# Optimization experiments

Measured on AMD Instinct MI355X. Metric: run time of the kernel, lower is better.

Reference implementation:

```python
import jax, jax.numpy as jnp
import numpy as np

T, N, D, E, L = 3, 50000, 64, 800000, 2


def setup_inputs() -> dict:
    key = jax.random.key(0)
    ks = jax.random.split(key, 12)
    glorot = lambda k, shape: jax.random.uniform(
        k, shape, jnp.float32, -1.0, 1.0) * np.sqrt(6.0 / (shape[-2] + shape[-1]))
    return {
        "x": jax.random.normal(ks[0], (N, D), jnp.float32),
        "edge_index": jax.random.randint(ks[1], (2, E), 0, N),
        "edge_type": jax.random.randint(ks[2], (E,), 0, T),
        "edge_feature": jax.random.normal(ks[3], (T, D), jnp.float32),
        # per-layer parameters stacked along leading L axis
        "theta_g": glorot(ks[4], (L, T, D)),
        "theta_hi": glorot(ks[5], (L, T, D)),
        "theta_hj": glorot(ks[6], (L, T, D)),
        "we": glorot(ks[7], (L, D, D)),
        "wr": glorot(ks[8], (L, D, D)),
    }


def _scatter_softmax(r, row, n):
    # r: [T,E], softmax over edges grouped by destination node `row`
    rT = r.T  # [E,T]
    m = jax.ops.segment_max(rT, row, num_segments=n)  # [N,T]
    e = jnp.exp(rT - m[row])
    s = jax.ops.segment_sum(e, row, num_segments=n)
    return (e / s[row]).T  # [T,E]


def _layer(x, ef, tg, thi, thj, we, wr, row, col, etype, n):
    # attention logits per edge, per type-slice
    r_g = jnp.einsum('ed,td->te', ef, tg)[:, etype]          # [T,E]
    r_hi = jnp.einsum('tnd,td->tn', x, thi)[:, row]          # [T,E]
    r_hj = jnp.einsum('tnd,td->tn', x, thj)[:, col]          # [T,E]
    r = _scatter_softmax(r_g + r_hi + r_hj, row, n)          # [T,E]
    ef_new = ef @ wr                                         # [et,D]
    v = jax.nn.sigmoid(ef_new)[etype][None] * (x @ we)[:, col]  # [T,E,D]
    out = r[..., None] * v                                   # [T,E,D]
    out = jax.ops.segment_sum(out.transpose(1, 0, 2), row, num_segments=n)
    return out.transpose(1, 0, 2), ef_new                    # [T,N,D]


def reference(x, edge_index, edge_type, edge_feature, theta_g, theta_hi, theta_hj, we, wr):
    row, col = edge_index[0], edge_index[1]
    h = jnp.broadcast_to(x[None], (T, N, D))
    ef = edge_feature
    for i in range(L):
        h_prev = h
        out, ef = _layer(h, ef, theta_g[i], theta_hi[i], theta_hj[i],
                         we[i], wr[i], row, col, edge_type, N)
        if i == L - 1:
            h = out
            break
        h = h_prev + jax.nn.relu(out)  # dropout p=0 -> identity
        ef = jax.nn.relu(ef)
    return h
```

## Files before the change

### kernel.cpp

```cpp
#include <hip/hip_runtime.h>
#include <math.h>

#define TT 3
#define NN 50000
#define DD 64
#define EE 800000
#define LL 2
#define NK3 (NN * TT)
#define CH 96
#define NBC ((EE + 255) / 256)
#define NBM ((NN + 63) / 64)
#define NBKT ((NN + 127) / 128)
#define KPB 384
#define HP 3136

typedef _Float16 h4 __attribute__((ext_vector_type(4)));
typedef float f4 __attribute__((ext_vector_type(4)));

__global__ __launch_bounds__(256) void k_fusedA(
    const int* __restrict__ row, const int* __restrict__ et,
    int* __restrict__ blockHistT,
    const float* __restrict__ x,
    const float* __restrict__ we,
    const float* __restrict__ thj,
    _Float16* __restrict__ hw0,
    float* __restrict__ ahj0,
    const float* __restrict__ ef0,
    const float* __restrict__ tg,
    const float* __restrict__ wr,
    float* __restrict__ rg,
    float* __restrict__ sig,
    _Float16* __restrict__ bf)
{
    __shared__ _Float16 Ah[64][68];
    __shared__ _Float16 Bt[80][68];
    __shared__ int lhist[NBKT];
    int b = blockIdx.x, tid = threadIdx.x;

    if (b < NBC) {
        for (int i = tid; i < NBKT; i += 256) lhist[i] = 0;
        __syncthreads();
        int e = b * 256 + tid;
        int bkt = row[e] >> 7;
        atomicAdd(&lhist[bkt], 1);
        __syncthreads();
        for (int i = tid; i < NBKT; i += 256)
            blockHistT[(size_t)i * HP + b] = lhist[i];
        return;
    }
    if (b < NBC + NBM) {
        long rbase = (long)(b - NBC) * 64;
        #pragma unroll
        for (int it = 0; it < 4; ++it) {
            int flat = (tid + it * 256) * 4;
            int r = flat >> 6, k = flat & 63;
            h4 hv = {};
            if (rbase + r < NN) {
                float4 v = *(const float4*)&x[(rbase + r) * 64 + k];
                hv = h4{ (_Float16)v.x, (_Float16)v.y, (_Float16)v.z, (_Float16)v.w };
            }
            *(h4*)&Ah[r][k] = hv;
        }
        for (int idx = tid; idx < 80 * 64; idx += 256) {
            int c = idx >> 6, k = idx & 63;
            float v = 0.f;
            if (c < 64) v = we[k * 64 + c];
            else if (c < 67) v = thj[(c - 64) * 64 + k];
            Bt[c][k] = (_Float16)v;
        }
        __syncthreads();
        int wid = tid >> 6, lane = tid & 63;
        int r16 = lane & 15, kq = lane >> 4;
        f4 acc[5] = {};
        #pragma unroll
        for (int ks = 0; ks < 4; ++ks) {
            int k0 = ks * 16 + kq * 4;
            h4 a = *(h4*)&Ah[wid * 16 + r16][k0];
            #pragma unroll
            for (int ct = 0; ct < 5; ++ct) {
                h4 bb = *(h4*)&Bt[ct * 16 + r16][k0];
                acc[ct] = __builtin_amdgcn_mfma_f32_16x16x16f16(a, bb, acc[ct], 0, 0, 0);
            }
        }
        #pragma unroll
        for (int j = 0; j < 4; ++j) {
            long g = rbase + wid * 16 + kq * 4 + j;
            if (g < NN) {
                #pragma unroll
                for (int ct = 0; ct < 4; ++ct)
                    hw0[g * 64 + ct * 16 + r16] = (_Float16)acc[ct][j];
                if (r16 < 3) ahj0[g * 4 + r16] = acc[4][j];
            }
        }
        return;
    }
    float* ef_l = (float*)&Ah[0][0];
    float* efn  = ef_l + TT * DD;
    for (int l = 0; l < LL; ++l)
        for (int idx = tid; idx < 80 * 64; idx += 256) {
            int c = idx >> 6, k = idx & 63;
            float v = 0.f;
            if (c < 64) v = we[l * 4096 + k * 64 + c];
            else if (c < 67) v = thj[l * 192 + (c - 64) * 64 + k];
            bf[l * 5120 + idx] = (_Float16)v;
        }
    if (tid < TT * DD) ef_l[tid] = ef0[tid];
    __syncthreads();
    for (int layer = 0; layer < LL; ++layer) {
        if (tid < TT * TT) {
            int t = tid / TT, tau = tid % TT;
            float s = 0.f;
            #pragma unroll
            for (int k = 0; k < DD; ++k)
                s += ef_l[tau * DD + k] * tg[layer * TT * DD + t * DD + k];
            rg[layer * TT * TT + tid] = s;
        }
        if (tid < TT * DD) {
            int tau = tid / DD, d = tid % DD;
            float s = 0.f;
            #pragma unroll
            for (int k = 0; k < DD; ++k)
                s += ef_l[tau * DD + k] * wr[layer * DD * DD + k * DD + d];
            efn[tid] = s;
            sig[layer * TT * DD + tid] = 1.f / (1.f + expf(-s));
        }
        __syncthreads();
        if (tid < TT * DD) ef_l[tid] = fmaxf(efn[tid], 0.f);
        __syncthreads();
    }
}

__global__ __launch_bounds__(256) void k_colscan(
    int* __restrict__ blockHistT, int* __restrict__ bucketTotal)
{
    __shared__ int sc[256];
    __shared__ int carryB;
    int j = blockIdx.x, tid = threadIdx.x;
    int* colp = blockHistT + (size_t)j * HP;
    if (tid == 0) carryB = 0;
    __syncthreads();
    for (int c0 = 0; c0 < NBC; c0 += 256) {
        int b = c0 + tid;
        int v = (b < NBC) ? colp[b] : 0;
        sc[tid] = v;
        __syncthreads();
        for (int off = 1; off < 256; off <<= 1) {
            int u = (tid >= off) ? sc[tid - off] : 0;
            __syncthreads();
            sc[tid] += u;
            __syncthreads();
        }
        int cb = carryB;
        if (b < NBC) colp[b] = cb + sc[tid] - v;
        __syncthreads();
        if (tid == 0) carryB = cb + sc[255];
        __syncthreads();
    }
    if (tid == 0) bucketTotal[j] = carryB;
}

__global__ __launch_bounds__(256) void k_bucket(
    const int* __restrict__ row, const int* __restrict__ et,
    const int* __restrict__ col,
    const int* __restrict__ bucketTotal,
    const int* __restrict__ blockOffT,
    unsigned* __restrict__ bucketed)
{
    __shared__ int lrank[NBKT];
    __shared__ int lbase[NBKT];
    __shared__ int sc[256];
    __shared__ int carryC;
    int b = blockIdx.x, tid = threadIdx.x;
    for (int i = tid; i < NBKT; i += 256) lrank[i] = 0;
    if (tid == 0) carryC = 0;
    __syncthreads();
    for (int c0 = 0; c0 < NBKT; c0 += 256) {
        int i = c0 + tid;
        int v = (i < NBKT) ? bucketTotal[i] : 0;
        sc[tid] = v;
        __syncthreads();
        for (int off = 1; off < 256; off <<= 1) {
            int u = (tid >= off) ? sc[tid - off] : 0;
            __syncthreads();
            sc[tid] += u;
            __syncthreads();
        }
        int cb = carryC;
        if (i < NBKT) lbase[i] = cb + sc[tid] - v;
        __syncthreads();
        if (tid == 0) carryC = cb + sc[255];
        __syncthreads();
    }
    int e = b * 256 + tid;
    int r = row[e], tt = et[e], c = col[e];
    int bkt = r >> 7;
    int kl = (r - (bkt << 7)) * 3 + tt;
    int rk = atomicAdd(&lrank[bkt], 1);
    int pos = lbase[bkt] + blockOffT[(size_t)bkt * HP + b] + rk;
    bucketed[pos] = ((unsigned)kl << 16) | (unsigned)c;
}

__global__ __launch_bounds__(256) void k_emit3(
    const unsigned* __restrict__ bucketed,
    const int* __restrict__ bucketTotal,
    int* __restrict__ csroff,
    unsigned short* __restrict__ pk)
{
    __shared__ int counts[KPB];
    __shared__ int csr[KPB];
    __shared__ int sc[256];
    __shared__ int carryS;
    int j = blockIdx.x, tid = threadIdx.x;
    int pp = 0;
    for (int i = tid; i < j; i += 256) pp += bucketTotal[i];
    sc[tid] = pp;
    __syncthreads();
    for (int off = 128; off >= 1; off >>= 1) {
        if (tid < off) sc[tid] += sc[tid + off];
        __syncthreads();
    }
    int base = sc[0];
    int tot = bucketTotal[j];
    __syncthreads();
    for (int k = tid; k < KPB; k += 256) counts[k] = 0;
    if (tid == 0) carryS = 0;
    __syncthreads();
    for (int i = tid; i < tot; i += 256) {
        int kl = (int)(bucketed[base + i] >> 16);
        atomicAdd(&counts[kl], 1);
    }
    __syncthreads();
    for (int c0 = 0; c0 < KPB; c0 += 256) {
        int k = c0 + tid;
        int v = (k < KPB) ? counts[k] : 0;
        sc[tid] = v;
        __syncthreads();
        for (int off = 1; off < 256; off <<= 1) {
            int u = (tid >= off) ? sc[tid - off] : 0;
            __syncthreads();
            sc[tid] += u;
            __syncthreads();
        }
        int cb = carryS;
        if (k < KPB) csr[k] = cb + sc[tid] - v;
        __syncthreads();
        if (tid == 0) carryS = cb + sc[255];
        __syncthreads();
    }
    for (int k = tid; k < KPB; k += 256) {
        int gk = j * KPB + k;
        if (gk <= NK3) csroff[gk] = base + csr[k];
    }
    for (int k = tid; k < KPB; k += 256) counts[k] = 0;
    __syncthreads();
    for (int i = tid; i < tot; i += 256) {
        unsigned rec = bucketed[base + i];
        int kl = (int)(rec >> 16);
        int rk = atomicAdd(&counts[kl], 1);
        pk[base + csr[kl] + rk] = (unsigned short)(rec & 0xFFFFu);
    }
}

__global__ __launch_bounds__(256) void k_mm1(
    const _Float16* __restrict__ h,
    const _Float16* __restrict__ Bf,
    _Float16* __restrict__ hw,
    float* __restrict__ ahj)
{
    __shared__ _Float16 Ah[64][68];
    __shared__ _Float16 Bt[80][68];
    int tid = threadIdx.x;
    long rbase = (long)blockIdx.x * 64;

    #pragma unroll
    for (int it = 0; it < 4; ++it) {
        int flat = (tid + it * 256) * 4;
        int r = flat >> 6, k = flat & 63;
        h4 hv = {};
        if (rbase + r < NK3) hv = *(const h4*)&h[(rbase + r) * 64 + k];
        *(h4*)&Ah[r][k] = hv;
    }
    for (int e4 = tid; e4 < 80 * 64 / 4; e4 += 256) {
        int idx = e4 * 4;
        *(h4*)&Bt[idx >> 6][idx & 63] = *(const h4*)&Bf[idx];
    }
    __syncthreads();

    int wid = tid >> 6, lane = tid & 63;
    int r16 = lane & 15, kq = lane >> 4;
    f4 acc[5] = {};
    #pragma unroll
    for (int ks = 0; ks < 4; ++ks) {
        int k0 = ks * 16 + kq * 4;
        h4 a = *(h4*)&Ah[wid * 16 + r16][k0];
        #pragma unroll
        for (int ct = 0; ct < 5; ++ct) {
            h4 b = *(h4*)&Bt[ct * 16 + r16][k0];
            acc[ct] = __builtin_amdgcn_mfma_f32_16x16x16f16(a, b, acc[ct], 0, 0, 0);
        }
    }
    #pragma unroll
    for (int j = 0; j < 4; ++j) {
        long g = rbase + wid * 16 + kq * 4 + j;
        if (g < NK3) {
            int t = (g >= 2L * NN) ? 2 : (g >= NN ? 1 : 0);
            long n = g - (long)t * NN;
            #pragma unroll
            for (int ct = 0; ct < 4; ++ct)
                hw[((size_t)n * 3 + t) * 64 + ct * 16 + r16] = (_Float16)acc[ct][j];
            if (r16 == t) ahj[n * 4 + t] = acc[4][j];
        }
    }
}

__global__ __launch_bounds__(256) void k_edge0(
    const int* __restrict__ off3,
    const unsigned short* __restrict__ pk,
    const float* __restrict__ rg_l,
    const float* __restrict__ sig_l,
    const float* __restrict__ ahj4,
    const _Float16* __restrict__ hw,
    const float* __restrict__ x,
    _Float16* __restrict__ outh)
{
    __shared__ uint4 ent[4][CH];
    int wid = threadIdx.x >> 6, lane = threadIdx.x & 63;
    int n = blockIdx.x * 4 + wid;
    int b3 = n * 3;
    int s0 = off3[b3], s1 = off3[b3 + 1], s2 = off3[b3 + 2], s3 = off3[b3 + 3];
    float r00 = rg_l[0], r01 = rg_l[1], r02 = rg_l[2];
    float r10 = rg_l[3], r11 = rg_l[4], r12 = rg_l[5];
    float r20 = rg_l[6], r21 = rg_l[7], r22 = rg_l[8];
    float sg0 = sig_l[lane], sg1 = sig_l[64 + lane], sg2 = sig_l[128 + lane];
    const char* hwb = (const char*)hw + (size_t)lane * 2;
    uint4* myent = ent[wid];
    float acc0 = 0.f, acc1 = 0.f, acc2 = 0.f;
    float ps0 = 0.f, ps1 = 0.f, ps2 = 0.f;

    for (int base = s0; base < s3; base += CH) {
        int cnt = s3 - base; if (cnt > CH) cnt = CH;
        for (int jj = lane; jj < cnt; jj += 64) {
            int ei = base + jj;
            int c = pk[ei];
            int tau = (ei >= s1) + (ei >= s2);
            float4 aj = *(const float4*)&ahj4[c * 4];
            float g0 = (tau == 0) ? r00 : ((tau == 1) ? r01 : r02);
            float g1 = (tau == 0) ? r10 : ((tau == 1) ? r11 : r12);
            float g2 = (tau == 0) ? r20 : ((tau == 1) ? r21 : r22);
            float p0 = __expf(g0 + aj.x);
            float p1 = __expf(g1 + aj.y);
            float p2 = __expf(g2 + aj.z);
            ps0 += p0; ps1 += p1; ps2 += p2;
            myent[jj] = make_uint4(((unsigned)c * 128u) | ((unsigned)tau << 26),
                                   __float_as_uint(p0), __float_as_uint(p1),
                                   __float_as_uint(p2));
        }
        asm volatile("s_waitcnt lgkmcnt(0)" ::: "memory");

#define AGG(J) { uint4 e = myent[J];                                           \
        unsigned ta = e.x >> 26;                                               \
        float sg = (ta == 0) ? sg0 : ((ta == 1) ? sg1 : sg2);                  \
        float sv = sg * (float)*(const _Float16*)(hwb + (e.x & 0x03FFFFFFu));  \
        acc0 = fmaf(__uint_as_float(e.y), sv, acc0);                           \
        acc1 = fmaf(__uint_as_float(e.z), sv, acc1);                           \
        acc2 = fmaf(__uint_as_float(e.w), sv, acc2); }
        int j = 0;
        for (; j + 4 <= cnt; j += 4) { AGG(j) AGG(j + 1) AGG(j + 2) AGG(j + 3) }
        for (; j < cnt; ++j) { AGG(j) }
#undef AGG
        asm volatile("s_waitcnt lgkmcnt(0)" ::: "memory");
    }
    #pragma unroll
    for (int off = 32; off >= 1; off >>= 1) {
        ps0 += __shfl_xor(ps0, off);
        ps1 += __shfl_xor(ps1, off);
        ps2 += __shfl_xor(ps2, off);
    }
    float o0 = 0.f, o1 = 0.f, o2 = 0.f;
    if (s3 > s0) { o0 = acc0 / ps0; o1 = acc1 / ps1; o2 = acc2 / ps2; }
    size_t oi = (size_t)n * 64 + lane;
    float xv = x[oi];
    outh[oi]                       = (_Float16)(xv + fmaxf(o0, 0.f));
    outh[oi + (size_t)NN * 64]     = (_Float16)(xv + fmaxf(o1, 0.f));
    outh[oi + (size_t)2 * NN * 64] = (_Float16)(xv + fmaxf(o2, 0.f));
}

__global__ __launch_bounds__(256) void k_edge1(
    const int* __restrict__ off3,
    const unsigned short* __restrict__ pk,
    const float* __restrict__ rg_l,
    const float* __restrict__ sig_l,
    const float* __restrict__ ahj4,
    const _Float16* __restrict__ hw,
    float* __restrict__ outf)
{
    __shared__ uint4 ent[4][CH];
    int wid = threadIdx.x >> 6, lane = threadIdx.x & 63;
    int n = blockIdx.x * 4 + wid;
    int b3 = n * 3;
    int s0 = off3[b3], s1 = off3[b3 + 1], s2 = off3[b3 + 2], s3 = off3[b3 + 3];
    float r00 = rg_l[0], r01 = rg_l[1], r02 = rg_l[2];
    float r10 = rg_l[3], r11 = rg_l[4], r12 = rg_l[5];
    float r20 = rg_l[6], r21 = rg_l[7], r22 = rg_l[8];
    float sg0 = sig_l[lane], sg1 = sig_l[64 + lane], sg2 = sig_l[128 + lane];
    const char* hwb = (const char*)hw + (size_t)lane * 2;
    uint4* myent = ent[wid];
    float acc0 = 0.f, acc1 = 0.f, acc2 = 0.f;
    float ps0 = 0.f, ps1 = 0.f, ps2 = 0.f;

    for (int base = s0; base < s3; base += CH) {
        int cnt = s3 - base; if (cnt > CH) cnt = CH;
        for (int jj = lane; jj < cnt; jj += 64) {
            int ei = base + jj;
            int c = pk[ei];
            int tau = (ei >= s1) + (ei >= s2);
            float4 aj = *(const float4*)&ahj4[c * 4];
            float g0 = (tau == 0) ? r00 : ((tau == 1) ? r01 : r02);
            float g1 = (tau == 0) ? r10 : ((tau == 1) ? r11 : r12);
            float g2 = (tau == 0) ? r20 : ((tau == 1) ? r21 : r22);
            float p0 = __expf(g0 + aj.x);
            float p1 = __expf(g1 + aj.y);
            float p2 = __expf(g2 + aj.z);
            ps0 += p0; ps1 += p1; ps2 += p2;
            myent[jj] = make_uint4(((unsigned)c * 384u) | ((unsigned)tau << 26),
                                   __float_as_uint(p0), __float_as_uint(p1),
                                   __float_as_uint(p2));
        }
        asm volatile("s_waitcnt lgkmcnt(0)" ::: "memory");

#define AGG(J) { uint4 e = myent[J];                                           \
        unsigned ta = e.x >> 26;                                               \
        float sg = (ta == 0) ? sg0 : ((ta == 1) ? sg1 : sg2);                  \
        const char* ptr = hwb + (e.x & 0x03FFFFFFu);                           \
        float v0 = (float)*(const _Float16*)(ptr);                             \
        float v1 = (float)*(const _Float16*)(ptr + 128);                       \
        float v2 = (float)*(const _Float16*)(ptr + 256);                       \
        acc0 = fmaf(__uint_as_float(e.y), sg * v0, acc0);                      \
        acc1 = fmaf(__uint_as_float(e.z), sg * v1, acc1);                      \
        acc2 = fmaf(__uint_as_float(e.w), sg * v2, acc2); }
        int j = 0;
        for (; j + 4 <= cnt; j += 4) { AGG(j) AGG(j + 1) AGG(j + 2) AGG(j + 3) }
        for (; j < cnt; ++j) { AGG(j) }
#undef AGG
        asm volatile("s_waitcnt lgkmcnt(0)" ::: "memory");
    }
    #pragma unroll
    for (int off = 32; off >= 1; off >>= 1) {
        ps0 += __shfl_xor(ps0, off);
        ps1 += __shfl_xor(ps1, off);
        ps2 += __shfl_xor(ps2, off);
    }
    float o0 = 0.f, o1 = 0.f, o2 = 0.f;
    if (s3 > s0) { o0 = acc0 / ps0; o1 = acc1 / ps1; o2 = acc2 / ps2; }
    size_t oi = (size_t)n * 64 + lane;
    outf[oi]                       = o0;
    outf[oi + (size_t)NN * 64]     = o1;
    outf[oi + (size_t)2 * NN * 64] = o2;
}

extern "C" void kernel_launch(void* const* d_in, const int* in_sizes, int n_in,
                              void* d_out, int out_size, void* d_ws, size_t ws_size,
                              hipStream_t stream)
{
    const float* x   = (const float*)d_in[0];
    const int*   ei  = (const int*)d_in[1];
    const int*   row = ei;
    const int*   col = ei + EE;
    const int*   et  = (const int*)d_in[2];
    const float* ef  = (const float*)d_in[3];
    const float* tg  = (const float*)d_in[4];
    const float* thj = (const float*)d_in[6];
    const float* we  = (const float*)d_in[7];
    const float* wr  = (const float*)d_in[8];
    float* out = (float*)d_out;
    _Float16* h1h = (_Float16*)d_out;

    _Float16* hw1 = (_Float16*)d_ws;
    _Float16* hw0 = hw1 + (size_t)NN * 3 * 64;
    float* ahj0 = (float*)(hw0 + (size_t)NN * 64);
    float* ahj1 = ahj0 + (size_t)NN * 4;
    float* rg   = ahj1 + (size_t)NN * 4;
    float* sig  = rg + LL * 9;
    _Float16* bfB = (_Float16*)(sig + LL * 192);
    int* csroff3 = (int*)(bfB + LL * 5120);
    int* bucketTotal = csroff3 + NK3 + 1;
    int* blockHistT  = bucketTotal + NBKT;
    unsigned* bucketed = (unsigned*)(blockHistT + (size_t)NBKT * HP);
    unsigned short* csrpk = (unsigned short*)(bucketed + EE);

    k_fusedA<<<NBC + NBM + 1, 256, 0, stream>>>(row, et, blockHistT,
                                                x, we, thj, hw0, ahj0,
                                                ef, tg, wr, rg, sig, bfB);
    k_colscan<<<NBKT, 256, 0, stream>>>(blockHistT, bucketTotal);
    k_bucket<<<NBC, 256, 0, stream>>>(row, et, col, bucketTotal, blockHistT,
                                      bucketed);
    k_emit3<<<NBKT, 256, 0, stream>>>(bucketed, bucketTotal, csroff3, csrpk);

    k_edge0<<<NN / 4, 256, 0, stream>>>(csroff3, csrpk, rg, sig, ahj0, hw0,
                                        x, h1h);
    k_mm1<<<(NK3 + 63) / 64, 256, 0, stream>>>(h1h, bfB + 5120, hw1, ahj1);
    k_edge1<<<NN / 4, 256, 0, stream>>>(csroff3, csrpk, rg + 9, sig + 192,
                                        ahj1, hw1, out);
}
```

Baseline: 170.3 us.

## Coarsen bucket-sort histogram and scatter to 256 blocks of 3125 edges

The histogram and bucket-scatter passes now run 256 blocks that each handle 3125 edges, instead of 3125 blocks handling 256 edges each. The per-block histogram table drops from 3125 to 256 columns per bucket, so the column scan becomes one 256-wide scan per bucket with no carry loop. This cuts the histogram memory traffic and the serial scan cost. In exchange, each block does more serial work, only 256 blocks run on a large GPU, and shared-memory atomics see more contention per block.

```diff
diff --git a/kernel.cpp b/kernel.cpp
--- a/kernel.cpp
+++ b/kernel.cpp
@@ -8,18 +8,19 @@
 #define LL 2
 #define NK3 (NN * TT)
 #define CH 96
-#define NBC ((EE + 255) / 256)
 #define NBM ((NN + 63) / 64)
 #define NBKT ((NN + 127) / 128)
 #define KPB 384
-#define HP 3136
+#define NB2 256
+#define EPB2 (EE / NB2)
+#define HP2 392
 
 typedef _Float16 h4 __attribute__((ext_vector_type(4)));
 typedef float f4 __attribute__((ext_vector_type(4)));
 
 __global__ __launch_bounds__(256) void k_fusedA(
     const int* __restrict__ row, const int* __restrict__ et,
-    int* __restrict__ blockHistT,
+    int* __restrict__ blockHist,
     const float* __restrict__ x,
     const float* __restrict__ we,
     const float* __restrict__ thj,
@@ -37,19 +38,19 @@
     __shared__ int lhist[NBKT];
     int b = blockIdx.x, tid = threadIdx.x;
 
-    if (b < NBC) {
+    if (b < NB2) {
         for (int i = tid; i < NBKT; i += 256) lhist[i] = 0;
         __syncthreads();
-        int e = b * 256 + tid;
-        int bkt = row[e] >> 7;
-        atomicAdd(&lhist[bkt], 1);
+        int e0 = b * EPB2;
+        for (int i = tid; i < EPB2; i += 256)
+            atomicAdd(&lhist[row[e0 + i] >> 7], 1);
         __syncthreads();
         for (int i = tid; i < NBKT; i += 256)
-            blockHistT[(size_t)i * HP + b] = lhist[i];
+            blockHist[b * HP2 + i] = lhist[i];
         return;
     }
-    if (b < NBC + NBM) {
-        long rbase = (long)(b - NBC) * 64;
+    if (b < NB2 + NBM) {
+        long rbase = (long)(b - NB2) * 64;
         #pragma unroll
         for (int it = 0; it < 4; ++it) {
             int flat = (tid + it * 256) * 4;
@@ -131,39 +132,28 @@
 }
 
 __global__ __launch_bounds__(256) void k_colscan(
-    int* __restrict__ blockHistT, int* __restrict__ bucketTotal)
+    int* __restrict__ blockHist, int* __restrict__ bucketTotal)
 {
     __shared__ int sc[256];
-    __shared__ int carryB;
     int j = blockIdx.x, tid = threadIdx.x;
-    int* colp = blockHistT + (size_t)j * HP;
-    if (tid == 0) carryB = 0;
-    __syncthreads();
-    for (int c0 = 0; c0 < NBC; c0 += 256) {
-        int b = c0 + tid;
-        int v = (b < NBC) ? colp[b] : 0;
-        sc[tid] = v;
-        __syncthreads();
-        for (int off = 1; off < 256; off <<= 1) {
-            int u = (tid >= off) ? sc[tid - off] : 0;
-            __syncthreads();
-            sc[tid] += u;
-            __syncthreads();
-        }
-        int cb = carryB;
-        if (b < NBC) colp[b] = cb + sc[tid] - v;
-        __syncthreads();
-        if (tid == 0) carryB = cb + sc[255];
-        __syncthreads();
-    }
-    if (tid == 0) bucketTotal[j] = carryB;
+    int v = blockHist[tid * HP2 + j];
+    sc[tid] = v;
+    __syncthreads();
+    for (int off = 1; off < 256; off <<= 1) {
+        int u = (tid >= off) ? sc[tid - off] : 0;
+        __syncthreads();
+        sc[tid] += u;
+        __syncthreads();
+    }
+    blockHist[tid * HP2 + j] = sc[tid] - v;
+    if (tid == 255) bucketTotal[j] = sc[255];
 }
 
 __global__ __launch_bounds__(256) void k_bucket(
     const int* __restrict__ row, const int* __restrict__ et,
     const int* __restrict__ col,
     const int* __restrict__ bucketTotal,
-    const int* __restrict__ blockOffT,
+    const int* __restrict__ blockOff,
     unsigned* __restrict__ bucketed)
 {
     __shared__ int lrank[NBKT];
@@ -191,13 +181,16 @@
         if (tid == 0) carryC = cb + sc[255];
         __syncthreads();
     }
-    int e = b * 256 + tid;
-    int r = row[e], tt = et[e], c = col[e];
-    int bkt = r >> 7;
-    int kl = (r - (bkt << 7)) * 3 + tt;
-    int rk = atomicAdd(&lrank[bkt], 1);
-    int pos = lbase[bkt] + blockOffT[(size_t)bkt * HP + b] + rk;
-    bucketed[pos] = ((unsigned)kl << 16) | (unsigned)c;
+    int e0 = b * EPB2;
+    for (int i = tid; i < EPB2; i += 256) {
+        int e = e0 + i;
+        int r = row[e], tt = et[e], c = col[e];
+        int bkt = r >> 7;
+        int kl = (r - (bkt << 7)) * 3 + tt;
+        int rk = atomicAdd(&lrank[bkt], 1);
+        int pos = lbase[bkt] + blockOff[b * HP2 + bkt] + rk;
+        bucketed[pos] = ((unsigned)kl << 16) | (unsigned)c;
+    }
 }
 
 __global__ __launch_bounds__(256) void k_emit3(
@@ -484,15 +477,15 @@
     _Float16* bfB = (_Float16*)(sig + LL * 192);
     int* csroff3 = (int*)(bfB + LL * 5120);
     int* bucketTotal = csroff3 + NK3 + 1;
-    int* blockHistT  = bucketTotal + NBKT;
-    unsigned* bucketed = (unsigned*)(blockHistT + (size_t)NBKT * HP);
+    int* blockHist   = bucketTotal + NBKT;
+    unsigned* bucketed = (unsigned*)(blockHist + (size_t)NB2 * HP2);
     unsigned short* csrpk = (unsigned short*)(bucketed + EE);
 
-    k_fusedA<<<NBC + NBM + 1, 256, 0, stream>>>(row, et, blockHistT,
+    k_fusedA<<<NB2 + NBM + 1, 256, 0, stream>>>(row, et, blockHist,
                                                 x, we, thj, hw0, ahj0,
                                                 ef, tg, wr, rg, sig, bfB);
-    k_colscan<<<NBKT, 256, 0, stream>>>(blockHistT, bucketTotal);
-    k_bucket<<<NBC, 256, 0, stream>>>(row, et, col, bucketTotal, blockHistT,
+    k_colscan<<<NBKT, 256, 0, stream>>>(blockHist, bucketTotal);
+    k_bucket<<<NB2, 256, 0, stream>>>(row, et, col, bucketTotal, blockHist,
                                       bucketed);
     k_emit3<<<NBKT, 256, 0, stream>>>(bucketed, bucketTotal, csroff3, csrpk);
 
```

Measured after the change: 146.4 us. 14.0% less time.
